# Kernel tuning notes

Hardware: AMD Instinct MI355X
Metric: run time of the kernel (lower is better)

The kernel has to match this reference:

```python
import jax, jax.numpy as jnp
import numpy as np

MARGIN = 1.0
N, D = 8192, 128
NUM_CLASSES = 1024


def setup_inputs() -> dict:
    key = jax.random.key(0)
    k1, k2, k3 = jax.random.split(key, 3)
    a = jax.random.normal(k1, (N, D), dtype=jnp.float32)
    b = jax.random.normal(k2, (N, D), dtype=jnp.float32)
    # L2-normalize embeddings (standard for metric learning; keeps exp() stable)
    a = a / jnp.linalg.norm(a, axis=1, keepdims=True)
    b = b / jnp.linalg.norm(b, axis=1, keepdims=True)
    labels = jax.random.randint(k3, (N,), 0, NUM_CLASSES, dtype=jnp.int64 if jax.config.jax_enable_x64 else jnp.int32)
    return {"a": a, "b": b, "labels": labels}


def reference(a, b, labels):
    # S[i, j] = a_i . b_j  -- full pairwise similarity, one GEMM
    S = a @ b.T  # [N, N]
    same = labels[:, None] == labels[None, :]  # [N, N]
    eye = jnp.eye(labels.shape[0], dtype=bool)
    pos_mask = same & ~eye          # ordered positive pairs (i != j, same label)
    neg_mask = ~same                # ordered negative pairs (labels differ)
    # V[i] = sum_k in neg(i) exp(margin + S[i, k])
    V = jnp.sum(jnp.where(neg_mask, jnp.exp(MARGIN + S), 0.0), axis=1)  # [N]
    # per positive pair (i, j): max(log(V_i + V_j) - S_ij, 0)^2
    hinge = jnp.maximum(jnp.log(V[:, None] + V[None, :]) - S, 0.0)
    comp = jnp.where(pos_mask, hinge * hinge, 0.0)
    num_pos = jnp.sum(pos_mask)
    loss = jnp.sum(comp) / (2.0 * num_pos.astype(S.dtype))
    return loss
```

## Files before the change

### kernel.cpp

```cpp
#include <hip/hip_runtime.h>

#define NN 8192
#define DD 128
#define MAXCLS 64
#define NCHUNK 8
#define NBLK 256
#define TPB  512
#define LOG2E 1.4426950408889634f
#define E1    2.718281828459045f

typedef __attribute__((ext_vector_type(8))) short bf16x8;
typedef __attribute__((ext_vector_type(4))) float f32x4;

#if __has_builtin(__builtin_amdgcn_exp2f)
#define EXP2F(x) __builtin_amdgcn_exp2f(x)
#else
#define EXP2F(x) exp2f(x)
#endif

__device__ __forceinline__ void load16_lds(const unsigned short* g, unsigned short* l) {
    __builtin_amdgcn_global_load_lds(
        (const __attribute__((address_space(1))) unsigned int*)g,
        (__attribute__((address_space(3))) unsigned int*)l,
        16, 0, 0);
}

__device__ __forceinline__ unsigned short f2bf(float x) {
    unsigned u = __float_as_uint(x);
    u = (u + 0x7FFFu + ((u >> 16) & 1u)) >> 16;
    return (unsigned short)u;
}

__device__ __forceinline__ void st_agent(float* p, float v) {
    __hip_atomic_store(p, v, __ATOMIC_RELAXED, __HIP_MEMORY_SCOPE_AGENT);
}
__device__ __forceinline__ void st_agent(int* p, int v) {
    __hip_atomic_store(p, v, __ATOMIC_RELAXED, __HIP_MEMORY_SCOPE_AGENT);
}
__device__ __forceinline__ void st_agent(unsigned int* p, unsigned int v) {
    __hip_atomic_store(p, v, __ATOMIC_RELAXED, __HIP_MEMORY_SCOPE_AGENT);
}
__device__ __forceinline__ void st_agent(unsigned long long* p, unsigned long long v) {
    __hip_atomic_store(p, v, __ATOMIC_RELAXED, __HIP_MEMORY_SCOPE_AGENT);
}
__device__ __forceinline__ unsigned int ld_agent(const unsigned int* p) {
    return __hip_atomic_load(p, __ATOMIC_RELAXED, __HIP_MEMORY_SCOPE_AGENT);
}

__device__ __forceinline__ int xcd_id() {
    return (int)(__builtin_amdgcn_s_getreg(20 | (0 << 6) | (31 << 11)) & 7u);
}

__device__ __forceinline__ void grid_sync(int* subcnt, int* root, unsigned int* gen,
                                          unsigned int* doneg, int relay, int myxcd,
                                          int sub) {
    __syncthreads();
    if (threadIdx.x == 0) {
        unsigned int g = ld_agent(gen);
        int v = __hip_atomic_fetch_add(&subcnt[sub * 32], 1,
                                       __ATOMIC_RELAXED, __HIP_MEMORY_SCOPE_AGENT);
        if (v == (NBLK / 8) - 1) {
            __hip_atomic_store(&subcnt[sub * 32], 0, __ATOMIC_RELAXED, __HIP_MEMORY_SCOPE_AGENT);
            int r = __hip_atomic_fetch_add(root, 1, __ATOMIC_RELAXED, __HIP_MEMORY_SCOPE_AGENT);
            if (r == 7) {
                __hip_atomic_store(root, 0, __ATOMIC_RELAXED, __HIP_MEMORY_SCOPE_AGENT);
                st_agent(gen, g + 1u);
            }
        }
        if (relay) {
            long long t0 = clock64();
            while (ld_agent(gen) == g) {
                __builtin_amdgcn_s_sleep(1);
                if (clock64() - t0 > (1LL << 24)) break;
            }
            st_agent(&doneg[myxcd * 32], g + 1u);
        } else {
            long long t1 = clock64();
            while ((int)(ld_agent(&doneg[myxcd * 32]) - (g + 1u)) < 0) {
                __builtin_amdgcn_s_sleep(1);
                if (clock64() - t1 > (1LL << 24)) break;
            }
        }
    }
    __syncthreads();
}

__global__ __launch_bounds__(TPB, 2) void ml_fused_kernel(
    const float* __restrict__ a, const float* __restrict__ b,
    const int* __restrict__ labels,
    unsigned short* __restrict__ abf, unsigned short* __restrict__ bbf,
    int* __restrict__ cnt, int* __restrict__ list,
    float* __restrict__ Vp,
    float* __restrict__ classLoss, int* __restrict__ classCnt,
    float* __restrict__ out,
    int* subcnt, int* root, unsigned int* gen,
    int* claim, unsigned int* doneg)
{
    __shared__ char SM[74240];
    unsigned short (*Bs)[128 * DD] = (unsigned short (*)[128 * DD])SM;
    float* red = (float*)(SM + 73728);

    const int tid = threadIdx.x;
    const int bid = blockIdx.x;
    const int sub = bid & 7;

    int relay = 0, myxcd = 0;
    if (tid == 0) {
        myxcd = xcd_id();
        relay = (__hip_atomic_fetch_add(&claim[myxcd * 32], 1,
                                        __ATOMIC_RELAXED, __HIP_MEMORY_SCOPE_AGENT) == 0);
    }

#pragma unroll
    for (int it = 0; it < 4; it++) {
        int t = it * (NBLK * TPB) + bid * TPB + tid;
        const float* src = a;
        unsigned short* dst = abf;
        int idx = t;
        float scale = LOG2E;
        if (t >= 262144) { src = b; dst = bbf; idx = t - 262144; scale = 1.0f; }
        float4 v = ((const float4*)src)[idx];
        ushort4 o;
        o.x = f2bf(v.x * scale); o.y = f2bf(v.y * scale);
        o.z = f2bf(v.z * scale); o.w = f2bf(v.w * scale);
        union { ushort4 v4; unsigned long long u; } cvt;
        cvt.v4 = o;
        st_agent(((unsigned long long*)dst) + idx, cvt.u);
        if (t < NN) {
            int c = labels[t];
            int p = atomicAdd(&cnt[c], 1);
            if (p < MAXCLS) st_agent(&list[c * MAXCLS + p], t);
        }
    }

    grid_sync(subcnt, root, gen, doneg, relay, myxcd, sub);

    {
        const int lane = tid & 63;
        const int wv   = tid >> 6;
        const int row0 = (bid >> 3) * 256;
        const int j0   = (bid & 7) * 1024;

        const int lr = lane >> 4;
        const int sp = lane & 15;
        const int m  = lane & 15;
        const int q  = lane >> 4;
        const int xr = m & 7;

#define STAGE128(SRCBASE, BUF)                                                         \
        _Pragma("unroll")                                                              \
        for (int i = 0; i < 4; i++) {                                                  \
            int rb = wv * 16 + i * 4;                                                  \
            int r  = rb + lr;                                                          \
            int cc = sp ^ (r & 7);                                                     \
            load16_lds(&(SRCBASE)[(size_t)r * DD + cc * 8], &Bs[BUF][rb * DD]);        \
        }

        STAGE128(&abf[(size_t)row0 * DD], 0);
        STAGE128(&bbf[(size_t)j0 * DD], 1);
        __syncthreads();

        const int wi = (wv >> 1) * 64;
        const int wj = (wv & 1) * 64;

        bf16x8 afr[4][4];
        if (wv < 4) {
#pragma unroll
            for (int ti = 0; ti < 4; ti++)
#pragma unroll
                for (int ks = 0; ks < 4; ks++) {
                    int r   = wi + ti * 16 + m;
                    int pos = (ks * 4 + q) ^ xr;
                    afr[ti][ks] = *(const bf16x8*)(&Bs[0][r * DD + pos * 8]);
                }
        }
        asm volatile("s_waitcnt lgkmcnt(0)" ::: "memory");
        __syncthreads();

        STAGE128(&abf[(size_t)(row0 + 128) * DD], 0);
        __syncthreads();
        if (wv >= 4) {
#pragma unroll
            for (int ti = 0; ti < 4; ti++)
#pragma unroll
                for (int ks = 0; ks < 4; ks++) {
                    int r   = (wi - 128) + ti * 16 + m;
                    int pos = (ks * 4 + q) ^ xr;
                    afr[ti][ks] = *(const bf16x8*)(&Bs[0][r * DD + pos * 8]);
                }
        }
        asm volatile("s_waitcnt lgkmcnt(0)" ::: "memory");
        __syncthreads();

        STAGE128(&bbf[(size_t)(j0 + 128) * DD], 0);

        float rs[4][4];
#pragma unroll
        for (int ti = 0; ti < 4; ti++)
#pragma unroll
            for (int rg = 0; rg < 4; rg++) rs[ti][rg] = 0.f;

        const f32x4 zero = {0.f, 0.f, 0.f, 0.f};
        f32x4 acc[4][4];

#define COMPUTE_TILE(BUF)                                                              \
        {                                                                              \
            __builtin_amdgcn_s_setprio(1);                                             \
            _Pragma("unroll")                                                          \
            for (int ks = 0; ks < 4; ks++) {                                           \
                bf16x8 bfr[4];                                                         \
                _Pragma("unroll")                                                      \
                for (int tj = 0; tj < 4; tj++) {                                       \
                    int r   = wj + tj * 16 + m;                                        \
                    int pos = (ks * 4 + q) ^ xr;                                       \
                    bfr[tj] = *(const bf16x8*)(&Bs[BUF][r * DD + pos * 8]);            \
                }                                                                      \
                _Pragma("unroll")                                                      \
                for (int ti = 0; ti < 4; ti++)                                         \
                    _Pragma("unroll")                                                  \
                    for (int tj = 0; tj < 4; tj++)                                     \
                        acc[ti][tj] = __builtin_amdgcn_mfma_f32_16x16x32_bf16(         \
                            afr[ti][ks], bfr[tj], (ks == 0) ? zero : acc[ti][tj],      \
                            0, 0, 0);                                                  \
            }                                                                          \
            __builtin_amdgcn_s_setprio(0);                                             \
        }

#define EPILOGUE()                                                                     \
        _Pragma("unroll")                                                              \
        for (int ti = 0; ti < 4; ti++)                                                 \
            _Pragma("unroll")                                                          \
            for (int tj = 0; tj < 4; tj++) {                                           \
                f32x4 c = acc[ti][tj];                                                 \
                rs[ti][0] += EXP2F(c[0]);                                              \
                rs[ti][1] += EXP2F(c[1]);                                              \
                rs[ti][2] += EXP2F(c[2]);                                              \
                rs[ti][3] += EXP2F(c[3]);                                              \
            }

#pragma unroll 2
        for (int jt = 0; jt < 6; jt++) {
            const int cb = (jt + 1) & 1;
            COMPUTE_TILE(cb);
            asm volatile("s_waitcnt lgkmcnt(0)" ::: "memory");
            __builtin_amdgcn_s_barrier();
            STAGE128(&bbf[(size_t)(j0 + (jt + 2) * 128) * DD], cb);
            EPILOGUE();
            asm volatile("s_waitcnt vmcnt(4)" ::: "memory");
            __builtin_amdgcn_s_barrier();
        }
        {
            COMPUTE_TILE(1);
            EPILOGUE();
            asm volatile("s_waitcnt vmcnt(0)" ::: "memory");
            __builtin_amdgcn_s_barrier();
        }
        {
            COMPUTE_TILE(0);
            EPILOGUE();
        }

#undef COMPUTE_TILE
#undef STAGE128
#undef EPILOGUE

#pragma unroll
        for (int ti = 0; ti < 4; ti++)
#pragma unroll
            for (int rg = 0; rg < 4; rg++) {
                float v = rs[ti][rg];
                v += __shfl_xor(v, 1);
                v += __shfl_xor(v, 2);
                v += __shfl_xor(v, 4);
                v += __shfl_xor(v, 8);
                rs[ti][rg] = v;
            }

        if ((wv & 1) == 1 && m == 0) {
#pragma unroll
            for (int ti = 0; ti < 4; ti++)
#pragma unroll
                for (int rg = 0; rg < 4; rg++)
                    red[(wv >> 1) * 64 + ti * 16 + q * 4 + rg] = rs[ti][rg];
        }
        __syncthreads();
        if ((wv & 1) == 0 && m == 0) {
#pragma unroll
            for (int ti = 0; ti < 4; ti++)
#pragma unroll
                for (int rg = 0; rg < 4; rg++) {
                    int rloc = ti * 16 + q * 4 + rg;
                    st_agent(&Vp[(size_t)(bid & 7) * NN + row0 + wi + rloc],
                             rs[ti][rg] + red[(wv >> 1) * 64 + rloc]);
                }
        }
    }

    grid_sync(subcnt, root, gen, doneg, relay, myxcd, sub);

    {
        char* sm = (char*)SM;
        const int h  = tid >> 7;
        const int ht = tid & 127;
        int*   memH    = (int*)  (sm + h * 18432);
        float* VadjH   = (float*)(sm + h * 18432 + 512);
        float* ScH     = (float*)(sm + h * 18432 + 1024);
        float* psH     = (float*)(sm + h * 18432 + 17408);
        int*   csH     = (int*)  (sm + h * 18432 + 17424);
        int*   mcs     = (int*)(sm + 73728);
        int*   cum     = (int*)(sm + 73744);

        const int c = bid * 4 + h;
        int mc = cnt[c];
        if (mc > MAXCLS) mc = MAXCLS;
        if (ht == 0) mcs[h] = mc;

        float vsum = 0.f;
        if (ht < mc) {
            int r = list[c * MAXCLS + ht];
            memH[ht] = r;
#pragma unroll
            for (int jc = 0; jc < NCHUNK; jc++) vsum += Vp[(size_t)jc * NN + r];
        }
        __syncthreads();
        if (tid == 0) {
            int s = 0;
#pragma unroll
            for (int k = 0; k < 4; k++) { cum[k] = s; s += mcs[k] * mcs[k]; }
            cum[4] = s;
        }
        __syncthreads();

        const int g = tid >> 4;
        const int l = tid & 15;
        const int tot = cum[4];
        for (int pp = g; pp < tot; pp += 32) {
            int k = (pp >= cum[2]) ? ((pp >= cum[3]) ? 3 : 2) : ((pp >= cum[1]) ? 1 : 0);
            int lp = pp - cum[k];
            int mck = mcs[k];
            int i = lp / mck;
            int j = lp - i * mck;
            int* memK = (int*)(sm + k * 18432);
            int ri = memK[i], rj = memK[j];
            const float4* ar = (const float4*)(a + (size_t)ri * DD) + l * 2;
            const float4* br = (const float4*)(b + (size_t)rj * DD) + l * 2;
            float4 a0 = ar[0], a1 = ar[1];
            float4 b0 = br[0], b1 = br[1];
            float s = 0.f;
            s = fmaf(a0.x, b0.x, s); s = fmaf(a0.y, b0.y, s);
            s = fmaf(a0.z, b0.z, s); s = fmaf(a0.w, b0.w, s);
            s = fmaf(a1.x, b1.x, s); s = fmaf(a1.y, b1.y, s);
            s = fmaf(a1.z, b1.z, s); s = fmaf(a1.w, b1.w, s);
            s += __shfl_xor(s, 1);
            s += __shfl_xor(s, 2);
            s += __shfl_xor(s, 4);
            s += __shfl_xor(s, 8);
            if (l == 0) ((float*)(sm + k * 18432 + 1024))[i * MAXCLS + j] = s;
        }
        __syncthreads();

        if (ht < mc) {
            float se = 0.f;
            for (int j = 0; j < mc; j++) se += __expf(ScH[ht * MAXCLS + j]);
            VadjH[ht] = E1 * (vsum - se);
        }
        __syncthreads();

        const int tot1 = mc * mc;
        float partial = 0.f;
        int   count   = 0;
        for (int pp = ht; pp < tot1; pp += 128) {
            int i = pp / mc;
            int j = pp - i * mc;
            if (i != j) {
                float hg = fmaxf(logf(VadjH[i] + VadjH[j]) - ScH[i * MAXCLS + j], 0.f);
                partial += hg * hg;
                count++;
            }
        }
        for (int off = 32; off > 0; off >>= 1) {
            partial += __shfl_down(partial, off);
            count   += __shfl_down(count, off);
        }
        if ((ht & 63) == 0) { psH[ht >> 6] = partial; csH[ht >> 6] = count; }
        __syncthreads();
        if (ht == 0) {
            st_agent(&classLoss[c], psH[0] + psH[1]);
            st_agent(&classCnt[c],  csH[0] + csH[1]);
        }
    }

    __syncthreads();
    __shared__ int amLast;
    if (tid == 0) {
        int last = 0;
        int v = __hip_atomic_fetch_add(&subcnt[sub * 32], 1,
                                       __ATOMIC_RELAXED, __HIP_MEMORY_SCOPE_AGENT);
        if (v == (NBLK / 8) - 1) {
            __hip_atomic_store(&subcnt[sub * 32], 0, __ATOMIC_RELAXED, __HIP_MEMORY_SCOPE_AGENT);
            int r = __hip_atomic_fetch_add(root, 1, __ATOMIC_RELAXED, __HIP_MEMORY_SCOPE_AGENT);
            if (r == 7) { __hip_atomic_store(root, 0, __ATOMIC_RELAXED, __HIP_MEMORY_SCOPE_AGENT); last = 1; }
        }
        amLast = last;
    }
    __syncthreads();
    if (amLast) {
        __shared__ double dred[8];
        __shared__ long long cred[8];
        const int lane = tid & 63, wvv = tid >> 6;
        double dls = 0.0;
        long long dct = 0;
        for (int k = tid; k < 1024; k += TPB) {
            dls += (double)__hip_atomic_load(&classLoss[k], __ATOMIC_RELAXED, __HIP_MEMORY_SCOPE_AGENT);
            dct += (long long)__hip_atomic_load(&classCnt[k], __ATOMIC_RELAXED, __HIP_MEMORY_SCOPE_AGENT);
        }
        for (int off = 32; off > 0; off >>= 1) {
            dls += __shfl_down(dls, off);
            dct += __shfl_down(dct, off);
        }
        if (lane == 0) { dred[wvv] = dls; cred[wvv] = dct; }
        __syncthreads();
        if (tid == 0) {
            double ls = 0.0;
            long long np = 0;
#pragma unroll
            for (int w = 0; w < 8; w++) { ls += dred[w]; np += cred[w]; }
            out[0] = (float)(ls / (2.0 * (double)np));
        }
    }
}

extern "C" void kernel_launch(void* const* d_in, const int* in_sizes, int n_in,
                              void* d_out, int out_size, void* d_ws, size_t ws_size,
                              hipStream_t stream)
{
    const float* a      = (const float*)d_in[0];
    const float* b      = (const float*)d_in[1];
    const int*   labels = (const int*)d_in[2];
    float* out = (float*)d_out;

    char* ws = (char*)d_ws;
    unsigned short* abf = (unsigned short*)ws;
    unsigned short* bbf = (unsigned short*)(ws + 2097152);
    char*     base2     = ws + 4194304;
    int*      cnt       = (int*)(base2);
    int*      subcnt    = (int*)(base2 + 4096);
    int*      root      = (int*)(base2 + 5120);
    unsigned int* gen   = (unsigned int*)(base2 + 5248);
    int*      claim     = (int*)(base2 + 5376);
    unsigned int* doneg = (unsigned int*)(base2 + 6400);
    float*    classLoss = (float*)(base2 + 8192);
    int*      classCnt  = (int*)(base2 + 12288);
    int*      list      = (int*)(base2 + 16384);
    float*    Vp        = (float*)(base2 + 278528);

    (void)hipMemsetAsync(cnt, 0, 8192, stream);

    ml_fused_kernel<<<NBLK, TPB, 0, stream>>>(
        a, b, labels, abf, bbf, cnt, list, Vp, classLoss, classCnt, out,
        subcnt, root, gen, claim, doneg);
}
```

Measured before the change: 107.9 us.

## Triple-buffer B tiles and interleave staging loads with MFMA k-steps

Grows LDS to three 32KB tile buffers so both A halves and the first B tile load together in one pass, removing two block-wide barriers in the prologue. The B-tile loop becomes a fully unrolled triple-buffered pipeline. Each k-step issues one slice of the next-next tile's global-to-LDS copy between its fragment reads and its MFMAs, so only one barrier per tile is needed. This spreads memory traffic across the compute and cuts synchronisation. In exchange, the larger LDS footprint (about 97KB per block) may reduce how many blocks fit per CU, and the full unroll increases code size.

```diff
diff --git a/kernel.cpp b/kernel.cpp
--- a/kernel.cpp
+++ b/kernel.cpp
@@ -96,9 +96,9 @@
     int* subcnt, int* root, unsigned int* gen,
     int* claim, unsigned int* doneg)
 {
-    __shared__ char SM[74240];
+    __shared__ char SM[98816];
     unsigned short (*Bs)[128 * DD] = (unsigned short (*)[128 * DD])SM;
-    float* red = (float*)(SM + 73728);
+    float* red = (float*)(SM + 98304);
 
     const int tid = threadIdx.x;
     const int bid = blockIdx.x;
@@ -147,52 +147,43 @@
         const int q  = lane >> 4;
         const int xr = m & 7;
 
-#define STAGE128(SRCBASE, BUF)                                                         \
-        _Pragma("unroll")                                                              \
-        for (int i = 0; i < 4; i++) {                                                  \
-            int rb = wv * 16 + i * 4;                                                  \
+#define STAGE1(SRCBASE, BUF, I)                                                        \
+        {                                                                              \
+            int rb = wv * 16 + (I) * 4;                                                \
             int r  = rb + lr;                                                          \
             int cc = sp ^ (r & 7);                                                     \
             load16_lds(&(SRCBASE)[(size_t)r * DD + cc * 8], &Bs[BUF][rb * DD]);        \
         }
-
-        STAGE128(&abf[(size_t)row0 * DD], 0);
-        STAGE128(&bbf[(size_t)j0 * DD], 1);
-        __syncthreads();
+#define STAGE128(SRCBASE, BUF)                                                         \
+        STAGE1(SRCBASE, BUF, 0) STAGE1(SRCBASE, BUF, 1)                                \
+        STAGE1(SRCBASE, BUF, 2) STAGE1(SRCBASE, BUF, 3)
+
+        STAGE128(&abf[(size_t)row0 * DD], 0)
+        STAGE128(&abf[(size_t)(row0 + 128) * DD], 1)
+        STAGE128(&bbf[(size_t)j0 * DD], 2)
+        asm volatile("s_waitcnt vmcnt(0)" ::: "memory");
+        __builtin_amdgcn_s_barrier();
 
         const int wi = (wv >> 1) * 64;
         const int wj = (wv & 1) * 64;
 
         bf16x8 afr[4][4];
-        if (wv < 4) {
+        {
+            const int abuf  = wv >> 2;
+            const int abase = wi - (abuf ? 128 : 0);
 #pragma unroll
             for (int ti = 0; ti < 4; ti++)
 #pragma unroll
                 for (int ks = 0; ks < 4; ks++) {
-                    int r   = wi + ti * 16 + m;
+                    int r   = abase + ti * 16 + m;
                     int pos = (ks * 4 + q) ^ xr;
-                    afr[ti][ks] = *(const bf16x8*)(&Bs[0][r * DD + pos * 8]);
+                    afr[ti][ks] = *(const bf16x8*)(&Bs[abuf][r * DD + pos * 8]);
                 }
         }
         asm volatile("s_waitcnt lgkmcnt(0)" ::: "memory");
-        __syncthreads();
-
-        STAGE128(&abf[(size_t)(row0 + 128) * DD], 0);
-        __syncthreads();
-        if (wv >= 4) {
-#pragma unroll
-            for (int ti = 0; ti < 4; ti++)
-#pragma unroll
-                for (int ks = 0; ks < 4; ks++) {
-                    int r   = (wi - 128) + ti * 16 + m;
-                    int pos = (ks * 4 + q) ^ xr;
-                    afr[ti][ks] = *(const bf16x8*)(&Bs[0][r * DD + pos * 8]);
-                }
-        }
-        asm volatile("s_waitcnt lgkmcnt(0)" ::: "memory");
-        __syncthreads();
-
-        STAGE128(&bbf[(size_t)(j0 + 128) * DD], 0);
+        __builtin_amdgcn_s_barrier();
+
+        STAGE128(&bbf[(size_t)(j0 + 128) * DD], 0)
 
         float rs[4][4];
 #pragma unroll
@@ -202,29 +193,6 @@
 
         const f32x4 zero = {0.f, 0.f, 0.f, 0.f};
         f32x4 acc[4][4];
-
-#define COMPUTE_TILE(BUF)                                                              \
-        {                                                                              \
-            __builtin_amdgcn_s_setprio(1);                                             \
-            _Pragma("unroll")                                                          \
-            for (int ks = 0; ks < 4; ks++) {                                           \
-                bf16x8 bfr[4];                                                         \
-                _Pragma("unroll")                                                      \
-                for (int tj = 0; tj < 4; tj++) {                                       \
-                    int r   = wj + tj * 16 + m;                                        \
-                    int pos = (ks * 4 + q) ^ xr;                                       \
-                    bfr[tj] = *(const bf16x8*)(&Bs[BUF][r * DD + pos * 8]);            \
-                }                                                                      \
-                _Pragma("unroll")                                                      \
-                for (int ti = 0; ti < 4; ti++)                                         \
-                    _Pragma("unroll")                                                  \
-                    for (int tj = 0; tj < 4; tj++)                                     \
-                        acc[ti][tj] = __builtin_amdgcn_mfma_f32_16x16x32_bf16(         \
-                            afr[ti][ks], bfr[tj], (ks == 0) ? zero : acc[ti][tj],      \
-                            0, 0, 0);                                                  \
-            }                                                                          \
-            __builtin_amdgcn_s_setprio(0);                                             \
-        }
 
 #define EPILOGUE()                                                                     \
         _Pragma("unroll")                                                              \
@@ -238,31 +206,53 @@
                 rs[ti][3] += EXP2F(c[3]);                                              \
             }
 
-#pragma unroll 2
-        for (int jt = 0; jt < 6; jt++) {
-            const int cb = (jt + 1) & 1;
-            COMPUTE_TILE(cb);
-            asm volatile("s_waitcnt lgkmcnt(0)" ::: "memory");
-            __builtin_amdgcn_s_barrier();
-            STAGE128(&bbf[(size_t)(j0 + (jt + 2) * 128) * DD], cb);
-            EPILOGUE();
-            asm volatile("s_waitcnt vmcnt(4)" ::: "memory");
-            __builtin_amdgcn_s_barrier();
-        }
-        {
-            COMPUTE_TILE(1);
-            EPILOGUE();
-            asm volatile("s_waitcnt vmcnt(0)" ::: "memory");
-            __builtin_amdgcn_s_barrier();
-        }
-        {
-            COMPUTE_TILE(0);
-            EPILOGUE();
-        }
-
-#undef COMPUTE_TILE
+#define TILE(JT, DOSTAGE)                                                              \
+        {                                                                              \
+            _Pragma("unroll")                                                          \
+            for (int ks = 0; ks < 4; ks++) {                                           \
+                bf16x8 bfr[4];                                                         \
+                _Pragma("unroll")                                                      \
+                for (int tj = 0; tj < 4; tj++) {                                       \
+                    int r   = wj + tj * 16 + m;                                        \
+                    int pos = (ks * 4 + q) ^ xr;                                       \
+                    bfr[tj] = *(const bf16x8*)(&Bs[((JT) + 2) % 3][r * DD + pos * 8]); \
+                }                                                                      \
+                if (DOSTAGE)                                                           \
+                    STAGE1(&bbf[(size_t)(j0 + ((JT) + 2) * 128) * DD],                 \
+                           ((JT) + 1) % 3, ks)                                         \
+                __builtin_amdgcn_s_setprio(1);                                         \
+                _Pragma("unroll")                                                      \
+                for (int ti = 0; ti < 4; ti++)                                         \
+                    _Pragma("unroll")                                                  \
+                    for (int tj = 0; tj < 4; tj++)                                     \
+                        acc[ti][tj] = __builtin_amdgcn_mfma_f32_16x16x32_bf16(         \
+                            afr[ti][ks], bfr[tj], (ks == 0) ? zero : acc[ti][tj],      \
+                            0, 0, 0);                                                  \
+                __builtin_amdgcn_s_setprio(0);                                         \
+            }                                                                          \
+            EPILOGUE()                                                                 \
+        }
+
+        TILE(0, 1)
+        asm volatile("s_waitcnt vmcnt(4)" ::: "memory"); __builtin_amdgcn_s_barrier();
+        TILE(1, 1)
+        asm volatile("s_waitcnt vmcnt(4)" ::: "memory"); __builtin_amdgcn_s_barrier();
+        TILE(2, 1)
+        asm volatile("s_waitcnt vmcnt(4)" ::: "memory"); __builtin_amdgcn_s_barrier();
+        TILE(3, 1)
+        asm volatile("s_waitcnt vmcnt(4)" ::: "memory"); __builtin_amdgcn_s_barrier();
+        TILE(4, 1)
+        asm volatile("s_waitcnt vmcnt(4)" ::: "memory"); __builtin_amdgcn_s_barrier();
+        TILE(5, 1)
+        asm volatile("s_waitcnt vmcnt(4)" ::: "memory"); __builtin_amdgcn_s_barrier();
+        TILE(6, 0)
+        asm volatile("s_waitcnt vmcnt(0)" ::: "memory"); __builtin_amdgcn_s_barrier();
+        TILE(7, 0)
+
+#undef TILE
+#undef EPILOGUE
 #undef STAGE128
-#undef EPILOGUE
+#undef STAGE1
 
 #pragma unroll
         for (int ti = 0; ti < 4; ti++)
```

Result: slower. 140.4 us (+30.2%).

## Triple-buffer B tiles in LDS and load both A halves at once

Applied to the files above, without the earlier changes.

Grows shared memory from two to three 128-row buffers. The A-fragment prologue now stages both A halves together with the first B tile before a single barrier, replacing the serialized multi-barrier sequence. The main loop uses a rotating three-buffer schedule, so the next B tile is issued before computing the current one and the mid-loop barrier is dropped. This lets loads overlap compute better, at the cost of higher LDS use (about 97KB per block), which may cut occupancy below the two blocks per CU the launch bounds ask for.

```diff
diff --git a/kernel.cpp b/kernel.cpp
--- a/kernel.cpp
+++ b/kernel.cpp
@@ -96,9 +96,9 @@
     int* subcnt, int* root, unsigned int* gen,
     int* claim, unsigned int* doneg)
 {
-    __shared__ char SM[74240];
+    __shared__ char SM[98816];
     unsigned short (*Bs)[128 * DD] = (unsigned short (*)[128 * DD])SM;
-    float* red = (float*)(SM + 73728);
+    float* red = (float*)(SM + 98304);
 
     const int tid = threadIdx.x;
     const int bid = blockIdx.x;
@@ -156,43 +156,32 @@
             load16_lds(&(SRCBASE)[(size_t)r * DD + cc * 8], &Bs[BUF][rb * DD]);        \
         }
 
-        STAGE128(&abf[(size_t)row0 * DD], 0);
-        STAGE128(&bbf[(size_t)j0 * DD], 1);
-        __syncthreads();
+        STAGE128(&abf[(size_t)row0 * DD], 0)
+        STAGE128(&abf[(size_t)(row0 + 128) * DD], 1)
+        STAGE128(&bbf[(size_t)j0 * DD], 2)
+        asm volatile("s_waitcnt vmcnt(0)" ::: "memory");
+        __builtin_amdgcn_s_barrier();
 
         const int wi = (wv >> 1) * 64;
         const int wj = (wv & 1) * 64;
 
         bf16x8 afr[4][4];
-        if (wv < 4) {
+        {
+            const int abuf  = wv >> 2;
+            const int abase = wi - (abuf ? 128 : 0);
 #pragma unroll
             for (int ti = 0; ti < 4; ti++)
 #pragma unroll
                 for (int ks = 0; ks < 4; ks++) {
-                    int r   = wi + ti * 16 + m;
+                    int r   = abase + ti * 16 + m;
                     int pos = (ks * 4 + q) ^ xr;
-                    afr[ti][ks] = *(const bf16x8*)(&Bs[0][r * DD + pos * 8]);
+                    afr[ti][ks] = *(const bf16x8*)(&Bs[abuf][r * DD + pos * 8]);
                 }
         }
         asm volatile("s_waitcnt lgkmcnt(0)" ::: "memory");
-        __syncthreads();
-
-        STAGE128(&abf[(size_t)(row0 + 128) * DD], 0);
-        __syncthreads();
-        if (wv >= 4) {
-#pragma unroll
-            for (int ti = 0; ti < 4; ti++)
-#pragma unroll
-                for (int ks = 0; ks < 4; ks++) {
-                    int r   = (wi - 128) + ti * 16 + m;
-                    int pos = (ks * 4 + q) ^ xr;
-                    afr[ti][ks] = *(const bf16x8*)(&Bs[0][r * DD + pos * 8]);
-                }
-        }
-        asm volatile("s_waitcnt lgkmcnt(0)" ::: "memory");
-        __syncthreads();
-
-        STAGE128(&bbf[(size_t)(j0 + 128) * DD], 0);
+        __builtin_amdgcn_s_barrier();
+
+        STAGE128(&bbf[(size_t)(j0 + 128) * DD], 0)
 
         float rs[4][4];
 #pragma unroll
@@ -238,31 +227,28 @@
                 rs[ti][3] += EXP2F(c[3]);                                              \
             }
 
-#pragma unroll 2
+#pragma unroll
         for (int jt = 0; jt < 6; jt++) {
-            const int cb = (jt + 1) & 1;
-            COMPUTE_TILE(cb);
-            asm volatile("s_waitcnt lgkmcnt(0)" ::: "memory");
-            __builtin_amdgcn_s_barrier();
-            STAGE128(&bbf[(size_t)(j0 + (jt + 2) * 128) * DD], cb);
-            EPILOGUE();
+            STAGE128(&bbf[(size_t)(j0 + (jt + 2) * 128) * DD], (jt + 1) % 3)
+            COMPUTE_TILE((jt + 2) % 3)
+            EPILOGUE()
             asm volatile("s_waitcnt vmcnt(4)" ::: "memory");
             __builtin_amdgcn_s_barrier();
         }
         {
-            COMPUTE_TILE(1);
-            EPILOGUE();
+            COMPUTE_TILE(2)
+            EPILOGUE()
             asm volatile("s_waitcnt vmcnt(0)" ::: "memory");
             __builtin_amdgcn_s_barrier();
         }
         {
-            COMPUTE_TILE(0);
-            EPILOGUE();
+            COMPUTE_TILE(0)
+            EPILOGUE()
         }
 
 #undef COMPUTE_TILE
+#undef EPILOGUE
 #undef STAGE128
-#undef EPILOGUE
 
 #pragma unroll
         for (int ti = 0; ti < 4; ti++)
```

New measurement: 141.4 us. 1.31x slower.
